# Kernel optimization log

Measured on AMD Instinct MI355X. Metric: run time of the kernel, lower is better.

## Reference

```python
import jax, jax.numpy as jnp
import numpy as np

B, D, L = 32768, 1024, 4

def setup_inputs() -> dict:
    key = jax.random.key(0)
    k1, k2, k3 = jax.random.split(key, 3)
    x = jax.random.normal(k1, (B, D), dtype=jnp.float32)
    # torch init: normal_(0, 0.005) for both weights and biases, shape (d,1) -> flatten to (d,)
    weights = jax.random.normal(k2, (L, D), dtype=jnp.float32) * 0.005
    biases = jax.random.normal(k3, (L, D), dtype=jnp.float32) * 0.005
    return {"x": x, "weights": weights, "biases": biases}

def reference(x, weights, biases):
    # DCN cross layer: x_{i+1} = x0 * (x_i . w_i) + b_i + x_i
    # Algebraically identical to matmul(bmm(x0, x_i^T), w_i) + b_i + x_i
    x0 = x  # [B, D]

    def step(cur, wb):
        w, b = wb  # [D], [D]
        s = cur @ w  # [B] scalar per row (x_i^T w_i)
        cur = x0 * s[:, None] + b[None, :] + cur  # [B, D]
        return cur, None

    out, _ = jax.lax.scan(step, x, (weights, biases))
    return out  # [B, D] (squeeze of [B, D, 1])
```

## Files before the change

kernel.cpp:

```cpp
#include <hip/hip_runtime.h>


#define DCN_D 1024
#define DCN_F4 (DCN_D / 4)


__global__ __launch_bounds__(256) void dcn_pre_kernel(
    const float* __restrict__ w,
    const float* __restrict__ b,
    float* __restrict__ ws)
{
    const int t = threadIdx.x;
    for (int d = t; d < DCN_D; d += 256)
        ws[d] = b[d] + b[DCN_D + d] + b[2 * DCN_D + d] + b[3 * DCN_D + d];
    float p[6] = {0, 0, 0, 0, 0, 0};
    for (int d = t; d < DCN_D; d += 256) {
        const float b0 = b[d], b1 = b[DCN_D + d], b2 = b[2 * DCN_D + d];
        const float w1 = w[DCN_D + d], w2 = w[2 * DCN_D + d], w3 = w[3 * DCN_D + d];
        p[0] = fmaf(b0, w1, p[0]);
        p[1] = fmaf(b0, w2, p[1]);
        p[2] = fmaf(b1, w2, p[2]);
        p[3] = fmaf(b0, w3, p[3]);
        p[4] = fmaf(b1, w3, p[4]);
        p[5] = fmaf(b2, w3, p[5]);
    }
    __shared__ float red[6][4];
    const int wave = t >> 6, lane = t & 63;
    #pragma unroll
    for (int k = 0; k < 6; ++k) {
        float v = p[k];
        #pragma unroll
        for (int off = 32; off > 0; off >>= 1) v += __shfl_down(v, off, 64);
        if (lane == 0) red[k][wave] = v;
    }
    __syncthreads();
    if (t < 6) ws[DCN_D + t] = red[t][0] + red[t][1] + red[t][2] + red[t][3];
}

__global__ __launch_bounds__(256) void dcn_main_kernel(
    const float* __restrict__ x,
    const float* __restrict__ w,
    const float* __restrict__ ws,
    float* __restrict__ out,
    int B)
{
    const int row  = (int)((blockIdx.x * 256u + threadIdx.x) >> 6);
    const int lane = threadIdx.x & 63;
    if (row >= B) return;

    const float4* __restrict__ xr = reinterpret_cast<const float4*>(x + (size_t)row * DCN_D);
    const float4* __restrict__ w4 = reinterpret_cast<const float4*>(w);

    float4 xv[4];
    float p0 = 0.f, p1 = 0.f, p2 = 0.f, p3 = 0.f;

    #pragma unroll
    for (int j = 0; j < 4; ++j) {
        const int idx = lane + 64 * j;
        const float4 xc = xr[idx];
        xv[j] = xc;
        const float4 w0 = w4[idx];
        const float4 w1 = w4[DCN_F4 + idx];
        const float4 w2 = w4[2 * DCN_F4 + idx];
        const float4 w3 = w4[3 * DCN_F4 + idx];
        p0 = fmaf(xc.x, w0.x, fmaf(xc.y, w0.y, fmaf(xc.z, w0.z, fmaf(xc.w, w0.w, p0))));
        p1 = fmaf(xc.x, w1.x, fmaf(xc.y, w1.y, fmaf(xc.z, w1.z, fmaf(xc.w, w1.w, p1))));
        p2 = fmaf(xc.x, w2.x, fmaf(xc.y, w2.y, fmaf(xc.z, w2.z, fmaf(xc.w, w2.w, p2))));
        p3 = fmaf(xc.x, w3.x, fmaf(xc.y, w3.y, fmaf(xc.z, w3.z, fmaf(xc.w, w3.w, p3))));
    }

    #pragma unroll
    for (int off = 1; off < 64; off <<= 1) {
        p0 += __shfl_xor(p0, off, 64);
        p1 += __shfl_xor(p1, off, 64);
        p2 += __shfl_xor(p2, off, 64);
        p3 += __shfl_xor(p3, off, 64);
    }

    const float c01 = ws[DCN_D + 0], c02 = ws[DCN_D + 1], c12 = ws[DCN_D + 2];
    const float c03 = ws[DCN_D + 3], c13 = ws[DCN_D + 4], c23 = ws[DCN_D + 5];
    const float s0 = p0;
    const float t1 = 1.f + s0;
    const float s1 = fmaf(p1, t1, c01);
    const float t2 = t1 + s1;
    const float s2 = fmaf(p2, t2, c02 + c12);
    const float t3 = t2 + s2;
    const float s3 = fmaf(p3, t3, c03 + c13 + c23);
    const float S  = t3 + s3;

    const float4* __restrict__ bs4 = reinterpret_cast<const float4*>(ws);
    float4* __restrict__ o4 = reinterpret_cast<float4*>(out + (size_t)row * DCN_D);
    #pragma unroll
    for (int j = 0; j < 4; ++j) {
        const int idx = lane + 64 * j;
        const float4 bb = bs4[idx];
        float4 o;
        o.x = fmaf(xv[j].x, S, bb.x);
        o.y = fmaf(xv[j].y, S, bb.y);
        o.z = fmaf(xv[j].z, S, bb.z);
        o.w = fmaf(xv[j].w, S, bb.w);
        o4[idx] = o;
    }
}

extern "C" void kernel_launch(void* const* d_in, const int* in_sizes, int n_in,
                              void* d_out, int out_size, void* d_ws, size_t ws_size,
                              hipStream_t stream) {
    const float* x = (const float*)d_in[0];
    const float* w = (const float*)d_in[1];
    const float* b = (const float*)d_in[2];
    float* out = (float*)d_out;
    float* ws = (float*)d_ws;
    const int B = in_sizes[0] / DCN_D;

    dcn_pre_kernel<<<1, 256, 0, stream>>>(w, b, ws);
    const int rows_per_block = 4;
    dcn_main_kernel<<<(B + rows_per_block - 1) / rows_per_block, 256, 0, stream>>>(
        x, w, ws, out, B);
}
```

Baseline: 51.38 us.

## Use persistent grid with register-cached weights and double-buffered row-pair loads

The main kernel becomes a persistent grid of 512 blocks. Each wave loads all four weight vectors and the summed bias once into registers, then walks row pairs in a grid-stride loop. While it computes and stores the current pair it prefetches the next pair into a second register buffer. This removes repeated weight and bias loads per row and overlaps memory latency, at the cost of much higher register pressure (about 64 float4 values held live), which may reduce occupancy or cause spills. Odd B would drop the last row.

```diff
diff --git a/kernel.cpp b/kernel.cpp
--- a/kernel.cpp
+++ b/kernel.cpp
@@ -44,63 +44,117 @@
     float* __restrict__ out,
     int B)
 {
-    const int row  = (int)((blockIdx.x * 256u + threadIdx.x) >> 6);
-    const int lane = threadIdx.x & 63;
-    if (row >= B) return;
+    const int wid  = (int)((blockIdx.x * blockDim.x + threadIdx.x) >> 6);
+    const int lane = (int)(threadIdx.x & 63);
+    const int nw   = (int)((gridDim.x * blockDim.x) >> 6);
+    const int npairs = B >> 1;
 
-    const float4* __restrict__ xr = reinterpret_cast<const float4*>(x + (size_t)row * DCN_D);
-    const float4* __restrict__ w4 = reinterpret_cast<const float4*>(w);
-
-    float4 xv[4];
-    float p0 = 0.f, p1 = 0.f, p2 = 0.f, p3 = 0.f;
-
+    const float4* __restrict__ w4  = reinterpret_cast<const float4*>(w);
+    const float4* __restrict__ bs4 = reinterpret_cast<const float4*>(ws);
+    float4 wv[4][4];
+    float4 bv[4];
     #pragma unroll
     for (int j = 0; j < 4; ++j) {
         const int idx = lane + 64 * j;
-        const float4 xc = xr[idx];
-        xv[j] = xc;
-        const float4 w0 = w4[idx];
-        const float4 w1 = w4[DCN_F4 + idx];
-        const float4 w2 = w4[2 * DCN_F4 + idx];
-        const float4 w3 = w4[3 * DCN_F4 + idx];
-        p0 = fmaf(xc.x, w0.x, fmaf(xc.y, w0.y, fmaf(xc.z, w0.z, fmaf(xc.w, w0.w, p0))));
-        p1 = fmaf(xc.x, w1.x, fmaf(xc.y, w1.y, fmaf(xc.z, w1.z, fmaf(xc.w, w1.w, p1))));
-        p2 = fmaf(xc.x, w2.x, fmaf(xc.y, w2.y, fmaf(xc.z, w2.z, fmaf(xc.w, w2.w, p2))));
-        p3 = fmaf(xc.x, w3.x, fmaf(xc.y, w3.y, fmaf(xc.z, w3.z, fmaf(xc.w, w3.w, p3))));
+        bv[j] = bs4[idx];
+        #pragma unroll
+        for (int l = 0; l < 4; ++l) wv[l][j] = w4[l * DCN_F4 + idx];
     }
+    const float c01   = ws[DCN_D + 0];
+    const float c2sum = ws[DCN_D + 1] + ws[DCN_D + 2];
+    const float c3sum = ws[DCN_D + 3] + ws[DCN_D + 4] + ws[DCN_D + 5];
 
-    #pragma unroll
-    for (int off = 1; off < 64; off <<= 1) {
-        p0 += __shfl_xor(p0, off, 64);
-        p1 += __shfl_xor(p1, off, 64);
-        p2 += __shfl_xor(p2, off, 64);
-        p3 += __shfl_xor(p3, off, 64);
+    int pair = wid;
+    if (pair >= npairs) return;
+
+    float4 xa[2][4], xb[2][4];
+
+#define LOADX(buf, pr) do {                                                          \
+    const float4* __restrict__ _x0 =                                                 \
+        reinterpret_cast<const float4*>(x + (size_t)(2 * (pr)) * DCN_D);             \
+    const float4* __restrict__ _x1 =                                                 \
+        reinterpret_cast<const float4*>(x + (size_t)(2 * (pr) + 1) * DCN_D);         \
+    _Pragma("unroll")                                                                \
+    for (int j = 0; j < 4; ++j) buf[0][j] = _x0[lane + 64 * j];                      \
+    _Pragma("unroll")                                                                \
+    for (int j = 0; j < 4; ++j) buf[1][j] = _x1[lane + 64 * j];                      \
+} while (0)
+
+#define COMPSTORE(buf, pr) do {                                                      \
+    float p0[4] = {0, 0, 0, 0}, p1[4] = {0, 0, 0, 0};                                \
+    _Pragma("unroll")                                                                \
+    for (int j = 0; j < 4; ++j) {                                                    \
+        _Pragma("unroll")                                                            \
+        for (int l = 0; l < 4; ++l) {                                                \
+            p0[l] = fmaf(buf[0][j].x, wv[l][j].x, fmaf(buf[0][j].y, wv[l][j].y,      \
+                    fmaf(buf[0][j].z, wv[l][j].z,                                    \
+                    fmaf(buf[0][j].w, wv[l][j].w, p0[l]))));                         \
+            p1[l] = fmaf(buf[1][j].x, wv[l][j].x, fmaf(buf[1][j].y, wv[l][j].y,      \
+                    fmaf(buf[1][j].z, wv[l][j].z,                                    \
+                    fmaf(buf[1][j].w, wv[l][j].w, p1[l]))));                         \
+        }                                                                            \
+    }                                                                                \
+    _Pragma("unroll")                                                                \
+    for (int off = 1; off < 64; off <<= 1) {                                         \
+        _Pragma("unroll")                                                            \
+        for (int l = 0; l < 4; ++l) {                                                \
+            p0[l] += __shfl_xor(p0[l], off, 64);                                     \
+            p1[l] += __shfl_xor(p1[l], off, 64);                                     \
+        }                                                                            \
+    }                                                                                \
+    const float t1a = 1.f + p0[0];                                                   \
+    const float s1a = fmaf(p0[1], t1a, c01);                                         \
+    const float t2a = t1a + s1a;                                                     \
+    const float s2a = fmaf(p0[2], t2a, c2sum);                                       \
+    const float t3a = t2a + s2a;                                                     \
+    const float s3a = fmaf(p0[3], t3a, c3sum);                                       \
+    const float S0  = t3a + s3a;                                                     \
+    const float t1b = 1.f + p1[0];                                                   \
+    const float s1b = fmaf(p1[1], t1b, c01);                                         \
+    const float t2b = t1b + s1b;                                                     \
+    const float s2b = fmaf(p1[2], t2b, c2sum);                                       \
+    const float t3b = t2b + s2b;                                                     \
+    const float s3b = fmaf(p1[3], t3b, c3sum);                                       \
+    const float S1  = t3b + s3b;                                                     \
+    float4* __restrict__ _o0 =                                                       \
+        reinterpret_cast<float4*>(out + (size_t)(2 * (pr)) * DCN_D);                 \
+    float4* __restrict__ _o1 =                                                       \
+        reinterpret_cast<float4*>(out + (size_t)(2 * (pr) + 1) * DCN_D);             \
+    _Pragma("unroll")                                                                \
+    for (int j = 0; j < 4; ++j) {                                                    \
+        const int idx = lane + 64 * j;                                               \
+        float4 a;                                                                    \
+        a.x = fmaf(buf[0][j].x, S0, bv[j].x);                                        \
+        a.y = fmaf(buf[0][j].y, S0, bv[j].y);                                        \
+        a.z = fmaf(buf[0][j].z, S0, bv[j].z);                                        \
+        a.w = fmaf(buf[0][j].w, S0, bv[j].w);                                        \
+        _o0[idx] = a;                                                                \
+        float4 c;                                                                    \
+        c.x = fmaf(buf[1][j].x, S1, bv[j].x);                                        \
+        c.y = fmaf(buf[1][j].y, S1, bv[j].y);                                        \
+        c.z = fmaf(buf[1][j].z, S1, bv[j].z);                                        \
+        c.w = fmaf(buf[1][j].w, S1, bv[j].w);                                        \
+        _o1[idx] = c;                                                                \
+    }                                                                                \
+} while (0)
+
+    LOADX(xa, pair);
+    int nxt = pair + nw;
+    #pragma unroll 1
+    for (;;) {
+        bool hn = nxt < npairs;
+        if (hn) LOADX(xb, nxt);
+        COMPSTORE(xa, pair);
+        if (!hn) break;
+        pair = nxt; nxt += nw;
+        hn = nxt < npairs;
+        if (hn) LOADX(xa, nxt);
+        COMPSTORE(xb, pair);
+        if (!hn) break;
+        pair = nxt; nxt += nw;
     }
-
-    const float c01 = ws[DCN_D + 0], c02 = ws[DCN_D + 1], c12 = ws[DCN_D + 2];
-    const float c03 = ws[DCN_D + 3], c13 = ws[DCN_D + 4], c23 = ws[DCN_D + 5];
-    const float s0 = p0;
-    const float t1 = 1.f + s0;
-    const float s1 = fmaf(p1, t1, c01);
-    const float t2 = t1 + s1;
-    const float s2 = fmaf(p2, t2, c02 + c12);
-    const float t3 = t2 + s2;
-    const float s3 = fmaf(p3, t3, c03 + c13 + c23);
-    const float S  = t3 + s3;
-
-    const float4* __restrict__ bs4 = reinterpret_cast<const float4*>(ws);
-    float4* __restrict__ o4 = reinterpret_cast<float4*>(out + (size_t)row * DCN_D);
-    #pragma unroll
-    for (int j = 0; j < 4; ++j) {
-        const int idx = lane + 64 * j;
-        const float4 bb = bs4[idx];
-        float4 o;
-        o.x = fmaf(xv[j].x, S, bb.x);
-        o.y = fmaf(xv[j].y, S, bb.y);
-        o.z = fmaf(xv[j].z, S, bb.z);
-        o.w = fmaf(xv[j].w, S, bb.w);
-        o4[idx] = o;
-    }
+#undef LOADX
+#undef COMPSTORE
 }
 
 extern "C" void kernel_launch(void* const* d_in, const int* in_sizes, int n_in,
@@ -114,7 +168,5 @@
     const int B = in_sizes[0] / DCN_D;
 
     dcn_pre_kernel<<<1, 256, 0, stream>>>(w, b, ws);
-    const int rows_per_block = 4;
-    dcn_main_kernel<<<(B + rows_per_block - 1) / rows_per_block, 256, 0, stream>>>(
-        x, w, ws, out, B);
+    dcn_main_kernel<<<512, 256, 0, stream>>>(x, w, ws, out, B);
 }
```

Result: slower. 53.23 us (+3.6%).

## Stage weights in LDS and double-buffer row-pair loads across waves

Applied to the files above, without the earlier changes.

Each wave now handles four pairs of rows instead of one row. The four weight vectors and the folded bias are staged once per block in shared memory, so they are no longer re-read from global/L2 for every row. Loads of the next row pair are issued before computing the current pair, double-buffering to overlap memory latency with compute and reduction. In exchange the kernel uses more registers and 20KB of LDS per block, and launches 8x fewer blocks, which may reduce occupancy and latency hiding in this memory-bound kernel. It also assumes B is even, since odd last rows are dropped.

```diff
diff --git a/kernel.cpp b/kernel.cpp
--- a/kernel.cpp
+++ b/kernel.cpp
@@ -3,6 +3,7 @@
 
 #define DCN_D 1024
 #define DCN_F4 (DCN_D / 4)
+#define PAIRS_PER_WAVE 4
 
 
 __global__ __launch_bounds__(256) void dcn_pre_kernel(
@@ -37,6 +38,10 @@
     if (t < 6) ws[DCN_D + t] = red[t][0] + red[t][1] + red[t][2] + red[t][3];
 }
 
+__device__ __forceinline__ float dot4acc(const float4 a, const float4 b, float acc) {
+    return fmaf(a.x, b.x, fmaf(a.y, b.y, fmaf(a.z, b.z, fmaf(a.w, b.w, acc))));
+}
+
 __global__ __launch_bounds__(256) void dcn_main_kernel(
     const float* __restrict__ x,
     const float* __restrict__ w,
@@ -44,63 +49,112 @@
     float* __restrict__ out,
     int B)
 {
-    const int row  = (int)((blockIdx.x * 256u + threadIdx.x) >> 6);
-    const int lane = threadIdx.x & 63;
-    if (row >= B) return;
+    __shared__ float4 w_lds[4 * DCN_F4];
+    __shared__ float4 b_lds[DCN_F4];
 
-    const float4* __restrict__ xr = reinterpret_cast<const float4*>(x + (size_t)row * DCN_D);
-    const float4* __restrict__ w4 = reinterpret_cast<const float4*>(w);
+    const int t      = (int)threadIdx.x;
+    const int lane   = t & 63;
+    const int wib    = t >> 6;
+    const int wid    = (int)blockIdx.x * 4 + wib;
+    const int npairs = B >> 1;
+    const int pair0  = wid * PAIRS_PER_WAVE;
 
-    float4 xv[4];
-    float p0 = 0.f, p1 = 0.f, p2 = 0.f, p3 = 0.f;
+    float4 xA[2][4], xB[2][4];
 
+#define LOADP(buf, pr) do {                                                      \
+    if ((pr) < npairs) {                                                         \
+        const float4* __restrict__ _x0 =                                         \
+            reinterpret_cast<const float4*>(x + (size_t)(2 * (pr)) * DCN_D);     \
+        const float4* __restrict__ _x1 =                                         \
+            reinterpret_cast<const float4*>(x + (size_t)(2 * (pr) + 1) * DCN_D); \
+        _Pragma("unroll")                                                        \
+        for (int j = 0; j < 4; ++j) buf[0][j] = _x0[lane + 64 * j];              \
+        _Pragma("unroll")                                                        \
+        for (int j = 0; j < 4; ++j) buf[1][j] = _x1[lane + 64 * j];              \
+    }                                                                            \
+} while (0)
+
+#define COMPP(buf, pr) do {                                                      \
+    if ((pr) < npairs) {                                                         \
+        float p0[4] = {0, 0, 0, 0}, p1[4] = {0, 0, 0, 0};                        \
+        _Pragma("unroll")                                                        \
+        for (int j = 0; j < 4; ++j) {                                            \
+            const int idx = lane + 64 * j;                                       \
+            _Pragma("unroll")                                                    \
+            for (int l = 0; l < 4; ++l) {                                        \
+                const float4 wv = w_lds[l * DCN_F4 + idx];                       \
+                p0[l] = dot4acc(buf[0][j], wv, p0[l]);                           \
+                p1[l] = dot4acc(buf[1][j], wv, p1[l]);                           \
+            }                                                                    \
+        }                                                                        \
+        _Pragma("unroll")                                                        \
+        for (int off = 1; off < 64; off <<= 1) {                                 \
+            _Pragma("unroll")                                                    \
+            for (int l = 0; l < 4; ++l) {                                        \
+                p0[l] += __shfl_xor(p0[l], off, 64);                             \
+                p1[l] += __shfl_xor(p1[l], off, 64);                             \
+            }                                                                    \
+        }                                                                        \
+        const float t1a = 1.f + p0[0];                                           \
+        const float s1a = fmaf(p0[1], t1a, c01);                                 \
+        const float t2a = t1a + s1a;                                             \
+        const float s2a = fmaf(p0[2], t2a, c2sum);                               \
+        const float t3a = t2a + s2a;                                             \
+        const float s3a = fmaf(p0[3], t3a, c3sum);                               \
+        const float S0  = t3a + s3a;                                             \
+        const float t1b = 1.f + p1[0];                                           \
+        const float s1b = fmaf(p1[1], t1b, c01);                                 \
+        const float t2b = t1b + s1b;                                             \
+        const float s2b = fmaf(p1[2], t2b, c2sum);                               \
+        const float t3b = t2b + s2b;                                             \
+        const float s3b = fmaf(p1[3], t3b, c3sum);                               \
+        const float S1  = t3b + s3b;                                             \
+        float4* __restrict__ _o0 =                                               \
+            reinterpret_cast<float4*>(out + (size_t)(2 * (pr)) * DCN_D);         \
+        float4* __restrict__ _o1 =                                               \
+            reinterpret_cast<float4*>(out + (size_t)(2 * (pr) + 1) * DCN_D);     \
+        _Pragma("unroll")                                                        \
+        for (int j = 0; j < 4; ++j) {                                            \
+            const int idx = lane + 64 * j;                                       \
+            const float4 bb = b_lds[idx];                                        \
+            float4 a;                                                            \
+            a.x = fmaf(buf[0][j].x, S0, bb.x);                                   \
+            a.y = fmaf(buf[0][j].y, S0, bb.y);                                   \
+            a.z = fmaf(buf[0][j].z, S0, bb.z);                                   \
+            a.w = fmaf(buf[0][j].w, S0, bb.w);                                   \
+            _o0[idx] = a;                                                        \
+            float4 c;                                                            \
+            c.x = fmaf(buf[1][j].x, S1, bb.x);                                   \
+            c.y = fmaf(buf[1][j].y, S1, bb.y);                                   \
+            c.z = fmaf(buf[1][j].z, S1, bb.z);                                   \
+            c.w = fmaf(buf[1][j].w, S1, bb.w);                                   \
+            _o1[idx] = c;                                                        \
+        }                                                                        \
+    }                                                                            \
+} while (0)
+
+    LOADP(xA, pair0);
+
+    const float4* __restrict__ w4  = reinterpret_cast<const float4*>(w);
+    const float4* __restrict__ bs4 = reinterpret_cast<const float4*>(ws);
     #pragma unroll
-    for (int j = 0; j < 4; ++j) {
-        const int idx = lane + 64 * j;
-        const float4 xc = xr[idx];
-        xv[j] = xc;
-        const float4 w0 = w4[idx];
-        const float4 w1 = w4[DCN_F4 + idx];
-        const float4 w2 = w4[2 * DCN_F4 + idx];
-        const float4 w3 = w4[3 * DCN_F4 + idx];
-        p0 = fmaf(xc.x, w0.x, fmaf(xc.y, w0.y, fmaf(xc.z, w0.z, fmaf(xc.w, w0.w, p0))));
-        p1 = fmaf(xc.x, w1.x, fmaf(xc.y, w1.y, fmaf(xc.z, w1.z, fmaf(xc.w, w1.w, p1))));
-        p2 = fmaf(xc.x, w2.x, fmaf(xc.y, w2.y, fmaf(xc.z, w2.z, fmaf(xc.w, w2.w, p2))));
-        p3 = fmaf(xc.x, w3.x, fmaf(xc.y, w3.y, fmaf(xc.z, w3.z, fmaf(xc.w, w3.w, p3))));
-    }
+    for (int i = 0; i < 4; ++i) w_lds[t + 256 * i] = w4[t + 256 * i];
+    b_lds[t] = bs4[t];
+    const float c01   = ws[DCN_D + 0];
+    const float c2sum = ws[DCN_D + 1] + ws[DCN_D + 2];
+    const float c3sum = ws[DCN_D + 3] + ws[DCN_D + 4] + ws[DCN_D + 5];
+    __syncthreads();
 
-    #pragma unroll
-    for (int off = 1; off < 64; off <<= 1) {
-        p0 += __shfl_xor(p0, off, 64);
-        p1 += __shfl_xor(p1, off, 64);
-        p2 += __shfl_xor(p2, off, 64);
-        p3 += __shfl_xor(p3, off, 64);
-    }
+    LOADP(xB, pair0 + 1);
+    COMPP(xA, pair0);
+    LOADP(xA, pair0 + 2);
+    COMPP(xB, pair0 + 1);
+    LOADP(xB, pair0 + 3);
+    COMPP(xA, pair0 + 2);
+    COMPP(xB, pair0 + 3);
 
-    const float c01 = ws[DCN_D + 0], c02 = ws[DCN_D + 1], c12 = ws[DCN_D + 2];
-    const float c03 = ws[DCN_D + 3], c13 = ws[DCN_D + 4], c23 = ws[DCN_D + 5];
-    const float s0 = p0;
-    const float t1 = 1.f + s0;
-    const float s1 = fmaf(p1, t1, c01);
-    const float t2 = t1 + s1;
-    const float s2 = fmaf(p2, t2, c02 + c12);
-    const float t3 = t2 + s2;
-    const float s3 = fmaf(p3, t3, c03 + c13 + c23);
-    const float S  = t3 + s3;
-
-    const float4* __restrict__ bs4 = reinterpret_cast<const float4*>(ws);
-    float4* __restrict__ o4 = reinterpret_cast<float4*>(out + (size_t)row * DCN_D);
-    #pragma unroll
-    for (int j = 0; j < 4; ++j) {
-        const int idx = lane + 64 * j;
-        const float4 bb = bs4[idx];
-        float4 o;
-        o.x = fmaf(xv[j].x, S, bb.x);
-        o.y = fmaf(xv[j].y, S, bb.y);
-        o.z = fmaf(xv[j].z, S, bb.z);
-        o.w = fmaf(xv[j].w, S, bb.w);
-        o4[idx] = o;
-    }
+#undef LOADP
+#undef COMPP
 }
 
 extern "C" void kernel_launch(void* const* d_in, const int* in_sizes, int n_in,
@@ -114,7 +168,7 @@
     const int B = in_sizes[0] / DCN_D;
 
     dcn_pre_kernel<<<1, 256, 0, stream>>>(w, b, ws);
-    const int rows_per_block = 4;
+    const int rows_per_block = 2 * PAIRS_PER_WAVE * 4;
     dcn_main_kernel<<<(B + rows_per_block - 1) / rows_per_block, 256, 0, stream>>>(
         x, w, ws, out, B);
 }
```

New measurement: 53.33 us. +3.8%, slower.
